# Kernel tuning notes

Measured on AMD Instinct MI355X. Metric: run time of the kernel, lower is better.

## Reference

```python
import jax, jax.numpy as jnp
import numpy as np

B, V, HP, WP = 1, 6, 37, 66
N, CD, CC = HP * WP, 768, 256
BEVH = BEVW = 100
Q = BEVH * BEVW
NH, NP, D, Z = 8, 4, 4, 8
HD = CC // NH
PC = (-51.2, -51.2, -5.0, 51.2, 51.2, 3.0)
SCALE, PT, PL = 0.5775, 0.0, 0.0
H2, W2 = 518, 924
EPS = 1e-6


def setup_inputs() -> dict:
    key = jax.random.key(0)
    ks = jax.random.split(key, 10)
    s = 0.02
    return {
        "last_tokens": jax.random.normal(ks[0], (B, V, N, CD), jnp.float32),
        "lidar2img": jax.random.normal(ks[1], (B, V, 4, 4), jnp.float32),
        "proj_w": jax.random.normal(ks[2], (CC, CD), jnp.float32) * s,
        "bev_query": jax.random.normal(ks[3], (Q, CC), jnp.float32) * s,
        "w_view": jnp.zeros((1, V, 1), jnp.float32),
        "vp_w": jax.random.normal(ks[4], (CC, CC), jnp.float32) * s,
        "vp_b": jnp.zeros((CC,), jnp.float32),
        "so_w": jax.random.normal(ks[5], (NH * NP * 2, CC), jnp.float32) * s,
        "so_b": jnp.zeros((NH * NP * 2,), jnp.float32),
        "aw_w": jax.random.normal(ks[6], (NH * NP, CC), jnp.float32) * s,
        "aw_b": jnp.zeros((NH * NP,), jnp.float32),
        "op_w": jax.random.normal(ks[7], (CC, CC), jnp.float32) * s,
        "op_b": jnp.zeros((CC,), jnp.float32),
    }


def _ref_points_3d():
    # normalized pillar reference points, (D, Q, 3) in xyz order, Q = h*BEVW + w
    xs = (jnp.arange(BEVW, dtype=jnp.float32) + 0.5) / BEVW
    ys = (jnp.arange(BEVH, dtype=jnp.float32) + 0.5) / BEVH
    zs = jnp.linspace(0.5, Z - 0.5, D, dtype=jnp.float32) / Z
    gx = jnp.broadcast_to(xs[None, :], (BEVH, BEVW)).reshape(-1)
    gy = jnp.broadcast_to(ys[:, None], (BEVH, BEVW)).reshape(-1)
    return jnp.stack([jnp.broadcast_to(gx, (D, Q)),
                      jnp.broadcast_to(gy, (D, Q)),
                      jnp.broadcast_to(zs[:, None], (D, Q))], axis=-1)


def reference(last_tokens, lidar2img, proj_w, bev_query, w_view,
              vp_w, vp_b, so_w, so_b, aw_w, aw_b, op_w, op_b):
    BV = B * V
    # ---- project 3D BEV pillar points to camera views ----
    ref = _ref_points_3d()  # (D, Q, 3)
    wx = ref[..., 0] * (PC[3] - PC[0]) + PC[0]
    wy = ref[..., 1] * (PC[4] - PC[1]) + PC[1]
    wz = ref[..., 2] * (PC[5] - PC[2]) + PC[2]
    ref4 = jnp.stack([wx, wy, wz, jnp.ones_like(wx)], axis=-1)  # (D, Q, 4)
    cam = jnp.einsum('bvij,dqj->bvdqi', lidar2img, ref4)  # (B, V, D, Q, 4)
    depth = cam[..., 2]
    bev_mask = depth > 1e-5
    uv = cam[..., :2] / jnp.clip(depth, 1e-5)[..., None]
    u = uv[..., 0] * SCALE + PL
    v = uv[..., 1] * SCALE + PT
    in_img = (u >= 0) & (u <= W2 - 1) & (v >= 0) & (v <= H2 - 1)
    valid = bev_mask & in_img
    refx = jnp.clip(u / max(W2 - 1.0, 1.0), 0.0, 1.0)
    refy = jnp.clip(v / max(H2 - 1.0, 1.0), 0.0, 1.0)
    w = jnp.maximum(valid.astype(jnp.float32), EPS)  # (B, V, D, Q)
    den = jnp.maximum(w.sum(2), EPS)
    rx = (refx * w).sum(2) / den
    ry = (refy * w).sum(2) / den
    ref2d = jnp.stack([rx, ry], axis=-1).reshape(BV, Q, 2)

    # ---- value features: 1x1 conv proj + value_proj ----
    val = jnp.einsum('bvnc,oc->bvno', last_tokens, proj_w).reshape(BV, N, CC)
    val = val @ vp_w.T + vp_b
    val = val.reshape(BV, N, NH, HD)

    # ---- deformable attention (single level) ----
    query = jnp.broadcast_to(bev_query[None], (BV, Q, CC))
    off = (query @ so_w.T + so_b).reshape(BV, Q, NH, NP, 2)
    attn = jax.nn.softmax((query @ aw_w.T + aw_b).reshape(BV, Q, NH, NP), axis=-1)
    normalizer = jnp.array([WP, HP], jnp.float32)
    loc = ref2d[:, :, None, None, :] + off / normalizer  # (BV, Q, NH, NP, 2)

    # bilinear sampling, grid_sample semantics (align_corners=False, zero pad)
    x = loc[..., 0] * WP - 0.5
    y = loc[..., 1] * HP - 0.5
    x0 = jnp.floor(x); y0 = jnp.floor(y)
    fx = x - x0; fy = y - y0
    x0i = x0.astype(jnp.int32); y0i = y0.astype(jnp.int32)
    b_idx = jnp.arange(BV)[:, None, None, None]
    h_idx = jnp.arange(NH)[None, None, :, None]

    def corner(xi, yi, wgt):
        ok = ((xi >= 0) & (xi < WP) & (yi >= 0) & (yi < HP)).astype(val.dtype)
        lin = jnp.clip(yi, 0, HP - 1) * WP + jnp.clip(xi, 0, WP - 1)
        g = val[b_idx, lin, h_idx]  # (BV, Q, NH, NP, HD)
        return g * (ok * wgt)[..., None]

    samp = (corner(x0i, y0i, (1 - fx) * (1 - fy))
            + corner(x0i + 1, y0i, fx * (1 - fy))
            + corner(x0i, y0i + 1, (1 - fx) * fy)
            + corner(x0i + 1, y0i + 1, fx * fy))
    out = (samp * attn[..., None]).sum(3).reshape(BV, Q, CC)
    out = out @ op_w.T + op_b + query  # residual (mmcv identity)

    # ---- view-weighted combine ----
    out = out.reshape(B, V, Q, CC)
    wv = jax.nn.softplus(w_view)  # (1, V, 1)
    num = (out * wv[..., None]).sum(1)  # (B, Q, CC)
    den_v = jnp.maximum(wv.sum(1), EPS)[..., None]
    bev = num / den_v
    return jnp.transpose(bev, (0, 2, 1)).reshape(B, CC, BEVH, BEVW)
```

## Files before the change

kernel.cpp:

```cpp
#include <hip/hip_runtime.h>
#include <math.h>

#define Q_TOT 10000
#define NVIEW 6
#define NTOK  2442
#define HP_   37
#define WP_   66
#define CD_   768
#define CC_   256

typedef __attribute__((ext_vector_type(8))) short bf16x8;
typedef __attribute__((ext_vector_type(4))) float f32x4;

__device__ inline unsigned f2bf(float f) {
    unsigned u = __builtin_bit_cast(unsigned, f);
    unsigned r = u + 0x7FFFu + ((u >> 16) & 1u);
    return r >> 16;
}

__global__ __launch_bounds__(256) void w2_kernel(const float* __restrict__ vp_w,
                                                 const float* __restrict__ proj_w,
                                                 unsigned short* __restrict__ W2b) {
    int b = blockIdx.x;
    int o2 = b / 3;
    int c = (b % 3) * 256 + threadIdx.x;
    __shared__ float vps[256];
    vps[threadIdx.x] = vp_w[(size_t)o2 * 256 + threadIdx.x];
    __syncthreads();
    float acc = 0.f;
#pragma unroll 16
    for (int o = 0; o < 256; ++o) {
        acc += vps[o] * proj_w[(size_t)o * CD_ + c];
    }
    W2b[(size_t)o2 * CD_ + c] = (unsigned short)f2bf(acc);
}

__global__ __launch_bounds__(256) void small_prep(const float* __restrict__ opw,
                                                  const float* __restrict__ l2i,
                                                  const float* __restrict__ so_w,
                                                  const float* __restrict__ so_b,
                                                  const float* __restrict__ aw_w,
                                                  const float* __restrict__ aw_b,
                                                  const float* __restrict__ wview,
                                                  unsigned short* __restrict__ opwb,
                                                  float* __restrict__ ref2d,
                                                  unsigned short* __restrict__ WQb,
                                                  float* __restrict__ bqp,
                                                  float* __restrict__ vwn) {
    int b = blockIdx.x, tid = threadIdx.x;
    if (b < 32) {
        int i = b * 256 + tid;
        float4 a = *(const float4*)(opw + (size_t)i * 8);
        float4 c4 = *(const float4*)(opw + (size_t)i * 8 + 4);
        uint4 o;
        o.x = f2bf(a.x) | (f2bf(a.y) << 16);
        o.y = f2bf(a.z) | (f2bf(a.w) << 16);
        o.z = f2bf(c4.x) | (f2bf(c4.y) << 16);
        o.w = f2bf(c4.z) | (f2bf(c4.w) << 16);
        *(uint4*)(opwb + (size_t)i * 8) = o;
    } else if (b < 267) {
        int idx = (b - 32) * 256 + tid;
        if (idx < NVIEW * Q_TOT) {
            int v = idx / Q_TOT, q = idx % Q_TOT;
            int wq = q % 100, hq = q / 100;
            float wx = (wq + 0.5f) * 1.024f - 51.2f;
            float wy = (hq + 0.5f) * 1.024f - 51.2f;
            const float* L = l2i + v * 16;
            float L0=L[0],L1=L[1],L2=L[2],L3=L[3],L4=L[4],L5=L[5],L6=L[6],L7=L[7];
            float L8=L[8],L9=L[9],L10=L[10],L11=L[11];
            float sw = 0.f, sx = 0.f, sy = 0.f;
#pragma unroll
            for (int d = 0; d < 4; ++d) {
                float zs = (0.5f + (float)d * (7.0f / 3.0f)) * 0.125f;
                float wz = zs * 8.0f - 5.0f;
                float c0 = L0 * wx + L1 * wy + L2 * wz + L3;
                float c1 = L4 * wx + L5 * wy + L6 * wz + L7;
                float c2 = L8 * wx + L9 * wy + L10 * wz + L11;
                bool bm = c2 > 1e-5f;
                float dc = fmaxf(c2, 1e-5f);
                float u  = (c0 / dc) * 0.5775f;
                float vv = (c1 / dc) * 0.5775f;
                bool in_img = (u >= 0.f) && (u <= 923.f) && (vv >= 0.f) && (vv <= 517.f);
                bool valid = bm && in_img;
                float refx = fminf(fmaxf(u / 923.0f, 0.f), 1.f);
                float refy = fminf(fmaxf(vv / 517.0f, 0.f), 1.f);
                float w = valid ? 1.0f : 1e-6f;
                sw += w; sx += refx * w; sy += refy * w;
            }
            float den = fmaxf(sw, 1e-6f);
            ref2d[(size_t)idx * 2 + 0] = sx / den;
            ref2d[(size_t)idx * 2 + 1] = sy / den;
        }
    } else {
        int row = b - 267, col = tid;
        float v = (row < 64) ? so_w[row * 256 + col] : (row < 96 ? aw_w[(row - 64) * 256 + col] : 0.f);
        WQb[row * 256 + col] = (unsigned short)f2bf(v);
        if (row == 0 && col < 128) bqp[col] = (col < 64) ? so_b[col] : (col < 96 ? aw_b[col - 64] : 0.f);
        if (row == 1 && col == 0) {
            float sp[6], swv = 0.f;
#pragma unroll
            for (int vv = 0; vv < NVIEW; ++vv) {
                float x = wview[vv];
                float s = (x > 20.f) ? x : log1pf(expf(x));
                sp[vv] = s; swv += s;
            }
            float inv = 1.0f / fmaxf(swv, 1e-6f);
#pragma unroll
            for (int vv = 0; vv < NVIEW; ++vv) vwn[vv] = sp[vv] * inv;
            vwn[6] = swv * inv;
            vwn[7] = 0.f;
        }
    }
}

template <int MODE, int KT>
__device__ __forceinline__ void gemm_body(char* base0, char* base1,
                                          const void* __restrict__ Aptr,
                                          const unsigned short* __restrict__ Bw,
                                          const float* __restrict__ bias,
                                          const float* __restrict__ resid,
                                          const float* __restrict__ wview,
                                          void* __restrict__ Cptr,
                                          int M, int nt_shift, int bid, int nwg) {
    constexpr int K = KT * 64;
    int tid = threadIdx.x;
    int wid = tid >> 6, lane = tid & 63;

    int qd = nwg >> 3, r = nwg & 7;
    int xcd = bid & 7, seq = bid >> 3;
    int wgid = (xcd < r) ? (xcd * (qd + 1) + seq) : (r * (qd + 1) + (xcd - r) * qd + seq);
    int mt = wgid >> nt_shift;
    int nt = wgid & ((1 << nt_shift) - 1);
    int m0 = mt * 64, n0 = nt * 64;

    int lr = lane & 15, lq = lane >> 4;
    int arow_s = tid >> 4;
    int ac4 = tid & 15;
    const float* Af = (const float*)Aptr;
    const unsigned short* Ah = (const unsigned short*)Aptr;
    float* Cf = (float*)Cptr;
    unsigned short* Ch = (unsigned short*)Cptr;

    f32x4 acc[4];
#pragma unroll
    for (int j = 0; j < 4; ++j) acc[j] = (f32x4)(0.f);

    float4 aF[2][4];
    uint4  aB[2][2];
    uint4  bR[2][2];
    const float4 zf4 = make_float4(0.f, 0.f, 0.f, 0.f);

#define LOADG(S, KTI) do {                                                            \
    int k0 = (KTI) << 6;                                                              \
    if (MODE == 0 || MODE == 2) {                                                     \
        _Pragma("unroll")                                                             \
        for (int p_ = 0; p_ < 4; ++p_) {                                              \
            int row_ = p_ * 16 + arow_s;                                              \
            bool av_ = (m0 + row_) < M;                                               \
            aF[S][p_] = av_ ? *(const float4*)(Af + (size_t)(m0 + row_) * K + k0 + ac4 * 4) : zf4; \
        }                                                                             \
    } else {                                                                          \
        _Pragma("unroll")                                                             \
        for (int i_ = 0; i_ < 2; ++i_) {                                              \
            int s_ = tid + (i_ << 8);                                                 \
            int row_ = s_ >> 3, c_ = s_ & 7;                                          \
            aB[S][i_] = *(const uint4*)(Ah + (size_t)(m0 + row_) * K + k0 + c_ * 8);  \
        }                                                                             \
    }                                                                                 \
    _Pragma("unroll")                                                                 \
    for (int i_ = 0; i_ < 2; ++i_) {                                                  \
        int s_ = tid + (i_ << 8);                                                     \
        int row_ = s_ >> 3, c_ = s_ & 7;                                              \
        bR[S][i_] = *(const uint4*)(Bw + (size_t)(n0 + row_) * K + k0 + c_ * 8);      \
    }                                                                                 \
} while (0)

#define TOLDS(S, PB) do {                                                             \
    char* Abb = (PB) ? base1 : base0;                                                 \
    if (MODE == 0 || MODE == 2) {                                                     \
        _Pragma("unroll")                                                             \
        for (int p_ = 0; p_ < 4; ++p_) {                                              \
            int row_ = p_ * 16 + arow_s;                                              \
            const float* f_ = (const float*)&aF[S][p_];                               \
            uint2 w_;                                                                 \
            w_.x = f2bf(f_[0]) | (f2bf(f_[1]) << 16);                                 \
            w_.y = f2bf(f_[2]) | (f2bf(f_[3]) << 16);                                 \
            int byte_ = row_ * 128 + (((ac4 >> 1) ^ (row_ & 7)) << 4) + ((ac4 & 1) << 3); \
            *(uint2*)(Abb + byte_) = w_;                                              \
        }                                                                             \
    } else {                                                                          \
        _Pragma("unroll")                                                             \
        for (int i_ = 0; i_ < 2; ++i_) {                                              \
            int s_ = tid + (i_ << 8);                                                 \
            int row_ = s_ >> 3, c_ = s_ & 7;                                          \
            *(uint4*)(Abb + row_ * 128 + ((c_ ^ (row_ & 7)) << 4)) = aB[S][i_];       \
        }                                                                             \
    }                                                                                 \
    char* Bbb = Abb + 8192;                                                           \
    _Pragma("unroll")                                                                 \
    for (int i_ = 0; i_ < 2; ++i_) {                                                  \
        int s_ = tid + (i_ << 8);                                                     \
        int row_ = s_ >> 3, c_ = s_ & 7;                                              \
        *(uint4*)(Bbb + row_ * 128 + ((c_ ^ (row_ & 7)) << 4)) = bR[S][i_];           \
    }                                                                                 \
} while (0)

#define MFMAS(PB) do {                                                                \
    char* Abb = (PB) ? base1 : base0;                                                 \
    char* Bbb = Abb + 8192;                                                           \
    _Pragma("unroll")                                                                 \
    for (int s_ = 0; s_ < 2; ++s_) {                                                  \
        int chunk_ = (s_ << 2) + lq;                                                  \
        int arow_ = (wid << 4) + lr;                                                  \
        bf16x8 af_ = *(bf16x8*)(Abb + arow_ * 128 + ((chunk_ ^ (arow_ & 7)) << 4));   \
        _Pragma("unroll")                                                             \
        for (int j_ = 0; j_ < 4; ++j_) {                                              \
            int brow_ = (j_ << 4) + lr;                                               \
            bf16x8 bf_ = *(bf16x8*)(Bbb + brow_ * 128 + ((chunk_ ^ (brow_ & 7)) << 4)); \
            acc[j_] = __builtin_amdgcn_mfma_f32_16x16x32_bf16(af_, bf_, acc[j_], 0, 0, 0); \
        }                                                                             \
    }                                                                                 \
} while (0)

#define BARRIER() do {                                                                \
    __builtin_amdgcn_sched_barrier(0);                                                \
    asm volatile("s_waitcnt lgkmcnt(0)" ::: "memory");                                \
    __builtin_amdgcn_s_barrier();                                                     \
    __builtin_amdgcn_sched_barrier(0);                                                \
} while (0)

    LOADG(0, 0);
#pragma unroll
    for (int kt = 0; kt < KT; ++kt) {
        if (kt + 1 < KT) LOADG((kt + 1) & 1, kt + 1);
        TOLDS(kt & 1, kt & 1);
        BARRIER();
        MFMAS(kt & 1);
    }

    int mb = m0 + (wid << 4) + (lq << 2);
    if (MODE == 0) {
#pragma unroll
        for (int j = 0; j < 4; ++j) {
            int n = n0 + (j << 4) + lr;
            float bn = bias[n];
#pragma unroll
            for (int e = 0; e < 4; ++e) {
                int m = mb + e;
                if (m < M) Ch[(size_t)m * 256 + n] = (unsigned short)f2bf(acc[j][e] + bn);
            }
        }
    } else if (MODE == 1) {
        float s = 0.f;
#pragma unroll
        for (int v = 0; v < 6; ++v) {
            float x = wview[v];
            s += (x > 20.f) ? x : log1pf(expf(x));
        }
        float f = s / fmaxf(s, 1e-6f);
#pragma unroll
        for (int j = 0; j < 4; ++j) {
            int n = n0 + (j << 4) + lr;
            float bn = bias[n];
            if (mb + 4 <= M) {
                float4 o;
                float* oo = (float*)&o;
#pragma unroll
                for (int e = 0; e < 4; ++e)
                    oo[e] = acc[j][e] + f * (bn + resid[(size_t)(mb + e) * 256 + n]);
                *(float4*)(Cf + (size_t)n * M + mb) = o;
            } else {
#pragma unroll
                for (int e = 0; e < 4; ++e) {
                    int m = mb + e;
                    if (m < M) Cf[(size_t)n * M + m] = acc[j][e] + f * (bn + resid[(size_t)m * 256 + n]);
                }
            }
        }
    } else {
#pragma unroll
        for (int j = 0; j < 4; ++j) {
            int n = n0 + (j << 4) + lr;
            if (n >= 96) continue;
            float bn = bias[n];
#pragma unroll
            for (int e = 0; e < 4; ++e) {
                int m = mb + e;
                if (m < M) Cf[(size_t)m * 96 + n] = acc[j][e] + bn;
            }
        }
    }
#undef LOADG
#undef TOLDS
#undef MFMAS
#undef BARRIER
}

__global__ __launch_bounds__(256, 4) void dual_gemm(const float* __restrict__ lt,
                                                    const unsigned short* __restrict__ W2b,
                                                    const float* __restrict__ vpb,
                                                    unsigned short* __restrict__ valB,
                                                    const float* __restrict__ bqq,
                                                    const unsigned short* __restrict__ WQb,
                                                    const float* __restrict__ bqp,
                                                    float* __restrict__ qout) {
    __shared__ unsigned short lds[4 * 64 * 64];
    char* b0 = (char*)lds;
    char* b1 = (char*)lds + 16384;
    if (blockIdx.x < 916)
        gemm_body<0, 12>(b0, b1, (const void*)lt, W2b, vpb, nullptr, nullptr,
                         (void*)valB, 14652, 2, blockIdx.x, 916);
    else
        gemm_body<2, 4>(b0, b1, (const void*)bqq, WQb, bqp, nullptr, nullptr,
                        (void*)qout, Q_TOT, 1, blockIdx.x - 916, 314);
}

__global__ __launch_bounds__(256, 4) void out_gemm(const unsigned short* __restrict__ sampavgB,
                                                   const unsigned short* __restrict__ opwb,
                                                   const float* __restrict__ opb,
                                                   const float* __restrict__ bqq,
                                                   const float* __restrict__ wview,
                                                   float* __restrict__ out) {
    __shared__ unsigned short lds[4 * 64 * 64];
    char* b0 = (char*)lds;
    char* b1 = (char*)lds + 16384;
    gemm_body<1, 4>(b0, b1, (const void*)sampavgB, opwb, opb, bqq, wview,
                    (void*)out, Q_TOT, 2, blockIdx.x, gridDim.x);
}

__global__ __launch_bounds__(256) void sample_kernel(const unsigned short* __restrict__ valB,
                                                     const float* __restrict__ ref2d,
                                                     const float* __restrict__ qout,
                                                     const float* __restrict__ vwn,
                                                     unsigned short* __restrict__ sampavgB) {
    __shared__ uint4  sOff[4 * 240];
    __shared__ float4 sW[4 * 240];
    __shared__ float4 sAt[4 * 8];
    __shared__ float  sVw[8];
    int tid = threadIdx.x;
    int qb = blockIdx.x * 4;

    if (tid < 32) {
        int ql = tid >> 3, h = tid & 7;
        const float* qo = qout + (size_t)(qb + ql) * 96 + 64 + h * 4;
        float a0 = qo[0], a1 = qo[1], a2 = qo[2], a3 = qo[3];
        float mx = fmaxf(fmaxf(a0, a1), fmaxf(a2, a3));
        float e0 = __expf(a0 - mx), e1 = __expf(a1 - mx), e2 = __expf(a2 - mx), e3 = __expf(a3 - mx);
        float inv = 1.0f / (e0 + e1 + e2 + e3);
        sAt[ql * 8 + h] = make_float4(e0 * inv, e1 * inv, e2 * inv, e3 * inv);
        if (tid < 8) sVw[tid] = vwn[tid < 6 ? tid : 0];
    }
    __syncthreads();

#pragma unroll
    for (int t = tid; t < 768; t += 256) {
        int ql = t / 192;
        int rem = t - ql * 192;
        int v = rem >> 5;
        int h = (rem >> 2) & 7;
        int p = rem & 3;
        int q = qb + ql;
        const float* qo = qout + (size_t)q * 96;
        float ox = qo[h * 8 + 2 * p];
        float oy = qo[h * 8 + 2 * p + 1];
        float at = ((const float*)&sAt[ql * 8 + h])[p];
        float scale = at * sVw[v];

        float rx = ref2d[(size_t)(v * Q_TOT + q) * 2 + 0];
        float ry = ref2d[(size_t)(v * Q_TOT + q) * 2 + 1];
        float x = rx * 66.0f + ox - 0.5f;
        float y = ry * 37.0f + oy - 0.5f;
        float xf = floorf(x), yf = floorf(y);
        float fx = x - xf, fy = y - yf;
        int xi = (int)xf, yi = (int)yf;

        float cw[4] = { (1.f - fx) * (1.f - fy), fx * (1.f - fy), (1.f - fx) * fy, fx * fy };
        unsigned off[4];
#pragma unroll
        for (int cyi = 0; cyi < 2; ++cyi) {
#pragma unroll
            for (int cxi = 0; cxi < 2; ++cxi) {
                int cx = xi + cxi, cy = yi + cyi;
                bool ok = (cx >= 0) && (cx < WP_) && (cy >= 0) && (cy < HP_);
                int ccx = cx < 0 ? 0 : (cx > WP_ - 1 ? WP_ - 1 : cx);
                int ccy = cy < 0 ? 0 : (cy > HP_ - 1 ? HP_ - 1 : cy);
                int c_ = cyi * 2 + cxi;
                off[c_] = (unsigned)((v * NTOK + ccy * WP_ + ccx) << 9);
                cw[c_] = ok ? cw[c_] * scale : 0.f;
            }
        }
        int slot = ql * 240 + v * 40 + h * 5 + p;
        sOff[slot] = make_uint4(off[0], off[1], off[2], off[3]);
        sW[slot]   = make_float4(cw[0], cw[1], cw[2], cw[3]);
    }
    __syncthreads();

    int ql = tid >> 6;
    int lane = tid & 63;
    int h = lane >> 3, d4 = (lane & 7) << 2;
    unsigned coff = (unsigned)((h * 32 + d4) << 1);
    const char* vbase = (const char*)valB;
    float acc0 = 0.f, acc1 = 0.f, acc2 = 0.f, acc3 = 0.f;
#pragma unroll
    for (int v = 0; v < NVIEW; ++v) {
#pragma unroll
        for (int p = 0; p < 4; ++p) {
            int slot = ql * 240 + v * 40 + h * 5 + p;
            uint4 off = sOff[slot];
            float4 w = sW[slot];
            uint2 r0 = *(const uint2*)(vbase + (off.x + coff));
            uint2 r1 = *(const uint2*)(vbase + (off.y + coff));
            uint2 r2 = *(const uint2*)(vbase + (off.z + coff));
            uint2 r3 = *(const uint2*)(vbase + (off.w + coff));
            float g0, g1;
            g0 = __builtin_bit_cast(float, r0.x << 16); g1 = __builtin_bit_cast(float, r0.x & 0xFFFF0000u);
            acc0 += w.x * g0; acc1 += w.x * g1;
            g0 = __builtin_bit_cast(float, r0.y << 16); g1 = __builtin_bit_cast(float, r0.y & 0xFFFF0000u);
            acc2 += w.x * g0; acc3 += w.x * g1;
            g0 = __builtin_bit_cast(float, r1.x << 16); g1 = __builtin_bit_cast(float, r1.x & 0xFFFF0000u);
            acc0 += w.y * g0; acc1 += w.y * g1;
            g0 = __builtin_bit_cast(float, r1.y << 16); g1 = __builtin_bit_cast(float, r1.y & 0xFFFF0000u);
            acc2 += w.y * g0; acc3 += w.y * g1;
            g0 = __builtin_bit_cast(float, r2.x << 16); g1 = __builtin_bit_cast(float, r2.x & 0xFFFF0000u);
            acc0 += w.z * g0; acc1 += w.z * g1;
            g0 = __builtin_bit_cast(float, r2.y << 16); g1 = __builtin_bit_cast(float, r2.y & 0xFFFF0000u);
            acc2 += w.z * g0; acc3 += w.z * g1;
            g0 = __builtin_bit_cast(float, r3.x << 16); g1 = __builtin_bit_cast(float, r3.x & 0xFFFF0000u);
            acc0 += w.w * g0; acc1 += w.w * g1;
            g0 = __builtin_bit_cast(float, r3.y << 16); g1 = __builtin_bit_cast(float, r3.y & 0xFFFF0000u);
            acc2 += w.w * g0; acc3 += w.w * g1;
        }
    }
    int q = qb + ql;
    unsigned u0 = f2bf(acc0) | (f2bf(acc1) << 16);
    unsigned u1 = f2bf(acc2) | (f2bf(acc3) << 16);
    *(uint2*)(sampavgB + (size_t)q * CC_ + h * 32 + d4) = make_uint2(u0, u1);
}

extern "C" void kernel_launch(void* const* d_in, const int* in_sizes, int n_in,
                              void* d_out, int out_size, void* d_ws, size_t ws_size,
                              hipStream_t stream) {
    const float* lt   = (const float*)d_in[0];
    const float* l2i  = (const float*)d_in[1];
    const float* proj = (const float*)d_in[2];
    const float* bqq  = (const float*)d_in[3];
    const float* wv   = (const float*)d_in[4];
    const float* vpw  = (const float*)d_in[5];
    const float* vpb  = (const float*)d_in[6];
    const float* sow  = (const float*)d_in[7];
    const float* sob  = (const float*)d_in[8];
    const float* aww  = (const float*)d_in[9];
    const float* awb  = (const float*)d_in[10];
    const float* opw  = (const float*)d_in[11];
    const float* opb  = (const float*)d_in[12];
    float* out = (float*)d_out;

    char* ws = (char*)d_ws;
    unsigned short* W2b   = (unsigned short*)(ws);
    unsigned short* opwb  = (unsigned short*)(ws + 393216);
    unsigned short* WQb   = (unsigned short*)(ws + 524288);
    float*          bqp   = (float*)(ws + 589824);
    float*          vwn   = (float*)(ws + 590336);
    float*          ref2d = (float*)(ws + 590848);
    float*          qout  = (float*)(ws + 1070848);
    unsigned short* valB  = (unsigned short*)(ws + 4910848);
    unsigned short* sampavgB = (unsigned short*)(ws + 12412672);

    hipLaunchKernelGGL(w2_kernel, dim3(768), dim3(256), 0, stream, vpw, proj, W2b);
    hipLaunchKernelGGL(small_prep, dim3(395), dim3(256), 0, stream,
                       opw, l2i, sow, sob, aww, awb, wv, opwb, ref2d, WQb, bqp, vwn);
    hipLaunchKernelGGL(dual_gemm, dim3(1230), dim3(256), 0, stream,
                       lt, W2b, vpb, valB, bqq, WQb, bqp, qout);
    hipLaunchKernelGGL(sample_kernel, dim3(Q_TOT / 4), dim3(256), 0, stream,
                       valB, ref2d, qout, vwn, sampavgB);
    hipLaunchKernelGGL(out_gemm, dim3(628), dim3(256), 0, stream,
                       sampavgB, opwb, opb, bqq, wv, out);
}
```

Baseline: 87.18 us.

## Use 128-row M tiles for the token projection GEMM in dual_gemm

```diff
diff --git a/kernel.cpp b/kernel.cpp
--- a/kernel.cpp
+++ b/kernel.cpp
@@ -113,6 +113,142 @@
     }
 }
 
+template <int KT>
+__device__ __forceinline__ void gemm_body128(char* base0, char* base1,
+                                             const float* __restrict__ Af,
+                                             const unsigned short* __restrict__ Bw,
+                                             const float* __restrict__ bias,
+                                             unsigned short* __restrict__ Ch,
+                                             int M, int bid, int nwg) {
+    constexpr int K = KT * 64;
+    int tid = threadIdx.x;
+    int wid = tid >> 6, lane = tid & 63;
+
+    int qd = nwg >> 3, r = nwg & 7;
+    int xcd = bid & 7, seq = bid >> 3;
+    int wgid = (xcd < r) ? (xcd * (qd + 1) + seq) : (r * (qd + 1) + (xcd - r) * qd + seq);
+    int mt = wgid >> 2;
+    int nt = wgid & 3;
+    int m0 = mt * 128, n0 = nt * 64;
+
+    int lr = lane & 15, lq = lane >> 4;
+    int arow_h = tid >> 2;
+    int af4 = (tid & 3) * 4;
+
+    f32x4 acc[2][4];
+#pragma unroll
+    for (int i = 0; i < 2; ++i)
+#pragma unroll
+        for (int j = 0; j < 4; ++j) acc[i][j] = (f32x4)(0.f);
+
+    float4 aF[2][2][4];
+    uint4  bR[2][2];
+    const float4 zf4 = make_float4(0.f, 0.f, 0.f, 0.f);
+
+#define LOADG1(S, KTI) do {                                                           \
+    int k0 = (KTI) << 6;                                                              \
+    _Pragma("unroll")                                                                 \
+    for (int p_ = 0; p_ < 2; ++p_) {                                                  \
+        int row_ = p_ * 64 + arow_h;                                                  \
+        bool av_ = (m0 + row_) < M;                                                   \
+        const float* ap = Af + (size_t)(m0 + row_) * K + k0 + af4 * 4;                \
+        aF[S][p_][0] = av_ ? *(const float4*)(ap + 0)  : zf4;                         \
+        aF[S][p_][1] = av_ ? *(const float4*)(ap + 4)  : zf4;                         \
+        aF[S][p_][2] = av_ ? *(const float4*)(ap + 8)  : zf4;                         \
+        aF[S][p_][3] = av_ ? *(const float4*)(ap + 12) : zf4;                         \
+    }                                                                                 \
+    _Pragma("unroll")                                                                 \
+    for (int i_ = 0; i_ < 2; ++i_) {                                                  \
+        int s_ = tid + (i_ << 8);                                                     \
+        int row_ = s_ >> 3, c_ = s_ & 7;                                              \
+        bR[S][i_] = *(const uint4*)(Bw + (size_t)(n0 + row_) * K + ((KTI) << 6) + c_ * 8); \
+    }                                                                                 \
+} while (0)
+
+#define TOLDS1(S, PB) do {                                                            \
+    char* Abb = (PB) ? base1 : base0;                                                 \
+    _Pragma("unroll")                                                                 \
+    for (int p_ = 0; p_ < 2; ++p_) {                                                  \
+        int row_ = p_ * 64 + arow_h;                                                  \
+        const float* f_ = (const float*)&aF[S][p_][0];                                \
+        unsigned u_[8];                                                               \
+        _Pragma("unroll")                                                             \
+        for (int k_ = 0; k_ < 4; ++k_) {                                              \
+            u_[2 * k_]     = f2bf(f_[4 * k_ + 0]) | (f2bf(f_[4 * k_ + 1]) << 16);     \
+            u_[2 * k_ + 1] = f2bf(f_[4 * k_ + 2]) | (f2bf(f_[4 * k_ + 3]) << 16);     \
+        }                                                                             \
+        int cb_ = (tid & 3) * 2;                                                      \
+        *(uint4*)(Abb + row_ * 128 + (((cb_) ^ (row_ & 7)) << 4))     = make_uint4(u_[0], u_[1], u_[2], u_[3]); \
+        *(uint4*)(Abb + row_ * 128 + (((cb_ + 1) ^ (row_ & 7)) << 4)) = make_uint4(u_[4], u_[5], u_[6], u_[7]); \
+    }                                                                                 \
+    char* Bbb = Abb + 16384;                                                          \
+    _Pragma("unroll")                                                                 \
+    for (int i_ = 0; i_ < 2; ++i_) {                                                  \
+        int s_ = tid + (i_ << 8);                                                     \
+        int row_ = s_ >> 3, c_ = s_ & 7;                                              \
+        *(uint4*)(Bbb + row_ * 128 + ((c_ ^ (row_ & 7)) << 4)) = bR[S][i_];           \
+    }                                                                                 \
+} while (0)
+
+#define MFMAS1(PB) do {                                                               \
+    char* Abb = (PB) ? base1 : base0;                                                 \
+    char* Bbb = Abb + 16384;                                                          \
+    _Pragma("unroll")                                                                 \
+    for (int s_ = 0; s_ < 2; ++s_) {                                                  \
+        int chunk_ = (s_ << 2) + lq;                                                  \
+        bf16x8 af0_, af1_;                                                            \
+        {                                                                             \
+            int ar0_ = (wid << 5) + lr;                                               \
+            int ar1_ = (wid << 5) + 16 + lr;                                          \
+            af0_ = *(bf16x8*)(Abb + ar0_ * 128 + ((chunk_ ^ (ar0_ & 7)) << 4));       \
+            af1_ = *(bf16x8*)(Abb + ar1_ * 128 + ((chunk_ ^ (ar1_ & 7)) << 4));       \
+        }                                                                             \
+        _Pragma("unroll")                                                             \
+        for (int j_ = 0; j_ < 4; ++j_) {                                              \
+            int brow_ = (j_ << 4) + lr;                                               \
+            bf16x8 bf_ = *(bf16x8*)(Bbb + brow_ * 128 + ((chunk_ ^ (brow_ & 7)) << 4)); \
+            acc[0][j_] = __builtin_amdgcn_mfma_f32_16x16x32_bf16(af0_, bf_, acc[0][j_], 0, 0, 0); \
+            acc[1][j_] = __builtin_amdgcn_mfma_f32_16x16x32_bf16(af1_, bf_, acc[1][j_], 0, 0, 0); \
+        }                                                                             \
+    }                                                                                 \
+} while (0)
+
+#define BARRIER1() do {                                                               \
+    __builtin_amdgcn_sched_barrier(0);                                                \
+    asm volatile("s_waitcnt lgkmcnt(0)" ::: "memory");                                \
+    __builtin_amdgcn_s_barrier();                                                     \
+    __builtin_amdgcn_sched_barrier(0);                                                \
+} while (0)
+
+    LOADG1(0, 0);
+#pragma unroll
+    for (int kt = 0; kt < KT; ++kt) {
+        if (kt + 1 < KT) LOADG1((kt + 1) & 1, kt + 1);
+        TOLDS1(kt & 1, kt & 1);
+        BARRIER1();
+        MFMAS1(kt & 1);
+    }
+
+#pragma unroll
+    for (int i = 0; i < 2; ++i) {
+        int mb = m0 + (wid << 5) + (i << 4) + (lq << 2);
+#pragma unroll
+        for (int j = 0; j < 4; ++j) {
+            int n = n0 + (j << 4) + lr;
+            float bn = bias[n];
+#pragma unroll
+            for (int e = 0; e < 4; ++e) {
+                int m = mb + e;
+                if (m < M) Ch[(size_t)m * 256 + n] = (unsigned short)f2bf(acc[i][j][e] + bn);
+            }
+        }
+    }
+#undef LOADG1
+#undef TOLDS1
+#undef MFMAS1
+#undef BARRIER1
+}
+
 template <int MODE, int KT>
 __device__ __forceinline__ void gemm_body(char* base0, char* base1,
                                           const void* __restrict__ Aptr,
@@ -139,7 +275,6 @@
     const float* Af = (const float*)Aptr;
     const unsigned short* Ah = (const unsigned short*)Aptr;
     float* Cf = (float*)Cptr;
-    unsigned short* Ch = (unsigned short*)Cptr;
 
     f32x4 acc[4];
 #pragma unroll
@@ -152,7 +287,7 @@
 
 #define LOADG(S, KTI) do {                                                            \
     int k0 = (KTI) << 6;                                                              \
-    if (MODE == 0 || MODE == 2) {                                                     \
+    if (MODE == 2) {                                                                  \
         _Pragma("unroll")                                                             \
         for (int p_ = 0; p_ < 4; ++p_) {                                              \
             int row_ = p_ * 16 + arow_s;                                              \
@@ -177,7 +312,7 @@
 
 #define TOLDS(S, PB) do {                                                             \
     char* Abb = (PB) ? base1 : base0;                                                 \
-    if (MODE == 0 || MODE == 2) {                                                     \
+    if (MODE == 2) {                                                                  \
         _Pragma("unroll")                                                             \
         for (int p_ = 0; p_ < 4; ++p_) {                                              \
             int row_ = p_ * 16 + arow_s;                                              \
@@ -239,18 +374,7 @@
     }
 
     int mb = m0 + (wid << 4) + (lq << 2);
-    if (MODE == 0) {
-#pragma unroll
-        for (int j = 0; j < 4; ++j) {
-            int n = n0 + (j << 4) + lr;
-            float bn = bias[n];
-#pragma unroll
-            for (int e = 0; e < 4; ++e) {
-                int m = mb + e;
-                if (m < M) Ch[(size_t)m * 256 + n] = (unsigned short)f2bf(acc[j][e] + bn);
-            }
-        }
-    } else if (MODE == 1) {
+    if (MODE == 1) {
         float s = 0.f;
 #pragma unroll
         for (int v = 0; v < 6; ++v) {
@@ -296,7 +420,7 @@
 #undef BARRIER
 }
 
-__global__ __launch_bounds__(256, 4) void dual_gemm(const float* __restrict__ lt,
+__global__ __launch_bounds__(256, 3) void dual_gemm(const float* __restrict__ lt,
                                                     const unsigned short* __restrict__ W2b,
                                                     const float* __restrict__ vpb,
                                                     unsigned short* __restrict__ valB,
@@ -304,15 +428,12 @@
                                                     const unsigned short* __restrict__ WQb,
                                                     const float* __restrict__ bqp,
                                                     float* __restrict__ qout) {
-    __shared__ unsigned short lds[4 * 64 * 64];
-    char* b0 = (char*)lds;
-    char* b1 = (char*)lds + 16384;
-    if (blockIdx.x < 916)
-        gemm_body<0, 12>(b0, b1, (const void*)lt, W2b, vpb, nullptr, nullptr,
-                         (void*)valB, 14652, 2, blockIdx.x, 916);
+    __shared__ char lds[49152];
+    if (blockIdx.x < 460)
+        gemm_body128<12>(lds, lds + 24576, lt, W2b, vpb, valB, 14652, blockIdx.x, 460);
     else
-        gemm_body<2, 4>(b0, b1, (const void*)bqq, WQb, bqp, nullptr, nullptr,
-                        (void*)qout, Q_TOT, 1, blockIdx.x - 916, 314);
+        gemm_body<2, 4>(lds, lds + 16384, (const void*)bqq, WQb, bqp, nullptr, nullptr,
+                        (void*)qout, Q_TOT, 1, blockIdx.x - 460, 314);
 }
 
 __global__ __launch_bounds__(256, 4) void out_gemm(const unsigned short* __restrict__ sampavgB,
@@ -321,10 +442,8 @@
                                                    const float* __restrict__ bqq,
                                                    const float* __restrict__ wview,
                                                    float* __restrict__ out) {
-    __shared__ unsigned short lds[4 * 64 * 64];
-    char* b0 = (char*)lds;
-    char* b1 = (char*)lds + 16384;
-    gemm_body<1, 4>(b0, b1, (const void*)sampavgB, opwb, opb, bqq, wview,
+    __shared__ char lds[32768];
+    gemm_body<1, 4>(lds, lds + 16384, (const void*)sampavgB, opwb, opb, bqq, wview,
                     (void*)out, Q_TOT, 2, blockIdx.x, gridDim.x);
 }
 
@@ -469,7 +588,7 @@
     hipLaunchKernelGGL(w2_kernel, dim3(768), dim3(256), 0, stream, vpw, proj, W2b);
     hipLaunchKernelGGL(small_prep, dim3(395), dim3(256), 0, stream,
                        opw, l2i, sow, sob, aww, awb, wv, opwb, ref2d, WQb, bqp, vwn);
-    hipLaunchKernelGGL(dual_gemm, dim3(1230), dim3(256), 0, stream,
+    hipLaunchKernelGGL(dual_gemm, dim3(774), dim3(256), 0, stream,
                        lt, W2b, vpb, valB, bqq, WQb, bqp, qout);
     hipLaunchKernelGGL(sample_kernel, dim3(Q_TOT / 4), dim3(256), 0, stream,
                        valB, ref2d, qout, vwn, sampavgB);
```

Result: slower. 158.9 us (+82.3%).

## Merge prep kernels and deepen GEMM global prefetch to three stages

Applied to the files above, without the earlier changes.

```diff
diff --git a/kernel.cpp b/kernel.cpp
--- a/kernel.cpp
+++ b/kernel.cpp
@@ -18,36 +18,37 @@
     return r >> 16;
 }
 
-__global__ __launch_bounds__(256) void w2_kernel(const float* __restrict__ vp_w,
-                                                 const float* __restrict__ proj_w,
-                                                 unsigned short* __restrict__ W2b) {
-    int b = blockIdx.x;
-    int o2 = b / 3;
-    int c = (b % 3) * 256 + threadIdx.x;
-    __shared__ float vps[256];
-    vps[threadIdx.x] = vp_w[(size_t)o2 * 256 + threadIdx.x];
-    __syncthreads();
-    float acc = 0.f;
+__global__ __launch_bounds__(256) void prep_all(const float* __restrict__ vp_w,
+                                                const float* __restrict__ proj_w,
+                                                const float* __restrict__ opw,
+                                                const float* __restrict__ l2i,
+                                                const float* __restrict__ so_w,
+                                                const float* __restrict__ so_b,
+                                                const float* __restrict__ aw_w,
+                                                const float* __restrict__ aw_b,
+                                                const float* __restrict__ wview,
+                                                unsigned short* __restrict__ W2b,
+                                                unsigned short* __restrict__ opwb,
+                                                float* __restrict__ ref2d,
+                                                unsigned short* __restrict__ WQb,
+                                                float* __restrict__ bqp,
+                                                float* __restrict__ vwn) {
+    int b0 = blockIdx.x, tid = threadIdx.x;
+    if (b0 < 768) {
+        int o2 = b0 / 3;
+        int c = (b0 % 3) * 256 + tid;
+        __shared__ float vps[256];
+        vps[tid] = vp_w[(size_t)o2 * 256 + tid];
+        __syncthreads();
+        float acc = 0.f;
 #pragma unroll 16
-    for (int o = 0; o < 256; ++o) {
-        acc += vps[o] * proj_w[(size_t)o * CD_ + c];
-    }
-    W2b[(size_t)o2 * CD_ + c] = (unsigned short)f2bf(acc);
-}
-
-__global__ __launch_bounds__(256) void small_prep(const float* __restrict__ opw,
-                                                  const float* __restrict__ l2i,
-                                                  const float* __restrict__ so_w,
-                                                  const float* __restrict__ so_b,
-                                                  const float* __restrict__ aw_w,
-                                                  const float* __restrict__ aw_b,
-                                                  const float* __restrict__ wview,
-                                                  unsigned short* __restrict__ opwb,
-                                                  float* __restrict__ ref2d,
-                                                  unsigned short* __restrict__ WQb,
-                                                  float* __restrict__ bqp,
-                                                  float* __restrict__ vwn) {
-    int b = blockIdx.x, tid = threadIdx.x;
+        for (int o = 0; o < 256; ++o) {
+            acc += vps[o] * proj_w[(size_t)o * CD_ + c];
+        }
+        W2b[(size_t)o2 * CD_ + c] = (unsigned short)f2bf(acc);
+        return;
+    }
+    int b = b0 - 768;
     if (b < 32) {
         int i = b * 256 + tid;
         float4 a = *(const float4*)(opw + (size_t)i * 8);
@@ -145,9 +146,9 @@
 #pragma unroll
     for (int j = 0; j < 4; ++j) acc[j] = (f32x4)(0.f);
 
-    float4 aF[2][4];
-    uint4  aB[2][2];
-    uint4  bR[2][2];
+    float4 aF[3][4];
+    uint4  aB[3][2];
+    uint4  bR[3][2];
     const float4 zf4 = make_float4(0.f, 0.f, 0.f, 0.f);
 
 #define LOADG(S, KTI) do {                                                            \
@@ -230,10 +231,12 @@
 } while (0)
 
     LOADG(0, 0);
+    if (KT > 1) LOADG(1, 1);
+    if (KT > 2) LOADG(2, 2);
 #pragma unroll
     for (int kt = 0; kt < KT; ++kt) {
-        if (kt + 1 < KT) LOADG((kt + 1) & 1, kt + 1);
-        TOLDS(kt & 1, kt & 1);
+        TOLDS(kt % 3, kt & 1);
+        if (kt + 3 < KT) LOADG(kt % 3, kt + 3);
         BARRIER();
         MFMAS(kt & 1);
     }
@@ -296,7 +299,7 @@
 #undef BARRIER
 }
 
-__global__ __launch_bounds__(256, 4) void dual_gemm(const float* __restrict__ lt,
+__global__ __launch_bounds__(256, 3) void dual_gemm(const float* __restrict__ lt,
                                                     const unsigned short* __restrict__ W2b,
                                                     const float* __restrict__ vpb,
                                                     unsigned short* __restrict__ valB,
@@ -315,7 +318,7 @@
                         (void*)qout, Q_TOT, 1, blockIdx.x - 916, 314);
 }
 
-__global__ __launch_bounds__(256, 4) void out_gemm(const unsigned short* __restrict__ sampavgB,
+__global__ __launch_bounds__(256, 3) void out_gemm(const unsigned short* __restrict__ sampavgB,
                                                    const unsigned short* __restrict__ opwb,
                                                    const float* __restrict__ opb,
                                                    const float* __restrict__ bqq,
@@ -466,9 +469,9 @@
     unsigned short* valB  = (unsigned short*)(ws + 4910848);
     unsigned short* sampavgB = (unsigned short*)(ws + 12412672);
 
-    hipLaunchKernelGGL(w2_kernel, dim3(768), dim3(256), 0, stream, vpw, proj, W2b);
-    hipLaunchKernelGGL(small_prep, dim3(395), dim3(256), 0, stream,
-                       opw, l2i, sow, sob, aww, awb, wv, opwb, ref2d, WQb, bqp, vwn);
+    hipLaunchKernelGGL(prep_all, dim3(1163), dim3(256), 0, stream,
+                       vpw, proj, opw, l2i, sow, sob, aww, awb, wv,
+                       W2b, opwb, ref2d, WQb, bqp, vwn);
     hipLaunchKernelGGL(dual_gemm, dim3(1230), dim3(256), 0, stream,
                        lt, W2b, vpb, valB, bqq, WQb, bqp, qout);
     hipLaunchKernelGGL(sample_kernel, dim3(Q_TOT / 4), dim3(256), 0, stream,
```

New measurement: 85.86 us. No clear change (-1.5%).

## Pre-convert tokens to bf16 and stage GEMM tiles via direct global-to-LDS loads

Applied to the files above, without the earlier changes.

```diff
diff --git a/kernel.cpp b/kernel.cpp
--- a/kernel.cpp
+++ b/kernel.cpp
@@ -18,38 +18,62 @@
     return r >> 16;
 }
 
-__global__ __launch_bounds__(256) void w2_kernel(const float* __restrict__ vp_w,
-                                                 const float* __restrict__ proj_w,
-                                                 unsigned short* __restrict__ W2b) {
-    int b = blockIdx.x;
-    int o2 = b / 3;
-    int c = (b % 3) * 256 + threadIdx.x;
-    __shared__ float vps[256];
-    vps[threadIdx.x] = vp_w[(size_t)o2 * 256 + threadIdx.x];
-    __syncthreads();
-    float acc = 0.f;
+__device__ __forceinline__ void glds16(const void* g, void* l) {
+    __builtin_amdgcn_global_load_lds(
+        (const __attribute__((address_space(1))) unsigned int*)g,
+        (__attribute__((address_space(3))) unsigned int*)l,
+        16, 0, 0);
+}
+
+__global__ __launch_bounds__(256) void prep_all(const float* __restrict__ lt,
+                                                const float* __restrict__ vp_w,
+                                                const float* __restrict__ proj_w,
+                                                const float* __restrict__ opw,
+                                                const float* __restrict__ l2i,
+                                                const float* __restrict__ so_w,
+                                                const float* __restrict__ so_b,
+                                                const float* __restrict__ aw_w,
+                                                const float* __restrict__ aw_b,
+                                                const float* __restrict__ wview,
+                                                unsigned short* __restrict__ ltB,
+                                                unsigned short* __restrict__ W2b,
+                                                unsigned short* __restrict__ opwb,
+                                                float* __restrict__ ref2d,
+                                                unsigned short* __restrict__ WQb,
+                                                float* __restrict__ bqp,
+                                                float* __restrict__ vwn) {
+    int b0 = blockIdx.x, tid = threadIdx.x;
+    if (b0 < 5495) {
+        int i = b0 * 256 + tid;
+        if (i < 1406592) {
+            float4 a = *(const float4*)(lt + (size_t)i * 8);
+            float4 c4 = *(const float4*)(lt + (size_t)i * 8 + 4);
+            uint4 o;
+            o.x = f2bf(a.x) | (f2bf(a.y) << 16);
+            o.y = f2bf(a.z) | (f2bf(a.w) << 16);
+            o.z = f2bf(c4.x) | (f2bf(c4.y) << 16);
+            o.w = f2bf(c4.z) | (f2bf(c4.w) << 16);
+            *(uint4*)(ltB + (size_t)i * 8) = o;
+        }
+        return;
+    }
+    if (b0 < 6263) {
+        int b = b0 - 5495;
+        int o2 = b / 3;
+        int c = (b % 3) * 256 + tid;
+        __shared__ float vps[256];
+        vps[tid] = vp_w[(size_t)o2 * 256 + tid];
+        __syncthreads();
+        float acc = 0.f;
 #pragma unroll 16
-    for (int o = 0; o < 256; ++o) {
-        acc += vps[o] * proj_w[(size_t)o * CD_ + c];
-    }
-    W2b[(size_t)o2 * CD_ + c] = (unsigned short)f2bf(acc);
-}
-
-__global__ __launch_bounds__(256) void small_prep(const float* __restrict__ opw,
-                                                  const float* __restrict__ l2i,
-                                                  const float* __restrict__ so_w,
-                                                  const float* __restrict__ so_b,
-                                                  const float* __restrict__ aw_w,
-                                                  const float* __restrict__ aw_b,
-                                                  const float* __restrict__ wview,
-                                                  unsigned short* __restrict__ opwb,
-                                                  float* __restrict__ ref2d,
-                                                  unsigned short* __restrict__ WQb,
-                                                  float* __restrict__ bqp,
-                                                  float* __restrict__ vwn) {
-    int b = blockIdx.x, tid = threadIdx.x;
-    if (b < 32) {
-        int i = b * 256 + tid;
+        for (int o = 0; o < 256; ++o) {
+            acc += vps[o] * proj_w[(size_t)o * CD_ + c];
+        }
+        W2b[(size_t)o2 * CD_ + c] = (unsigned short)f2bf(acc);
+        return;
+    }
+    if (b0 < 6295) {
+        int i = (b0 - 6263) * 256 + tid;
         float4 a = *(const float4*)(opw + (size_t)i * 8);
         float4 c4 = *(const float4*)(opw + (size_t)i * 8 + 4);
         uint4 o;
@@ -58,8 +82,10 @@
         o.z = f2bf(c4.x) | (f2bf(c4.y) << 16);
         o.w = f2bf(c4.z) | (f2bf(c4.w) << 16);
         *(uint4*)(opwb + (size_t)i * 8) = o;
-    } else if (b < 267) {
-        int idx = (b - 32) * 256 + tid;
+        return;
+    }
+    if (b0 < 6530) {
+        int idx = (b0 - 6295) * 256 + tid;
         if (idx < NVIEW * Q_TOT) {
             int v = idx / Q_TOT, q = idx % Q_TOT;
             int wq = q % 100, hq = q / 100;
@@ -91,8 +117,10 @@
             ref2d[(size_t)idx * 2 + 0] = sx / den;
             ref2d[(size_t)idx * 2 + 1] = sy / den;
         }
-    } else {
-        int row = b - 267, col = tid;
+        return;
+    }
+    {
+        int row = b0 - 6530, col = tid;
         float v = (row < 64) ? so_w[row * 256 + col] : (row < 96 ? aw_w[(row - 64) * 256 + col] : 0.f);
         WQb[row * 256 + col] = (unsigned short)f2bf(v);
         if (row == 0 && col < 128) bqp[col] = (col < 64) ? so_b[col] : (col < 96 ? aw_b[col - 64] : 0.f);
@@ -114,8 +142,8 @@
 }
 
 template <int MODE, int KT>
-__device__ __forceinline__ void gemm_body(char* base0, char* base1,
-                                          const void* __restrict__ Aptr,
+__device__ __forceinline__ void gemm_glds(char* base0, char* base1,
+                                          const unsigned short* __restrict__ Ah,
                                           const unsigned short* __restrict__ Bw,
                                           const float* __restrict__ bias,
                                           const float* __restrict__ resid,
@@ -134,10 +162,6 @@
     int m0 = mt * 64, n0 = nt * 64;
 
     int lr = lane & 15, lq = lane >> 4;
-    int arow_s = tid >> 4;
-    int ac4 = tid & 15;
-    const float* Af = (const float*)Aptr;
-    const unsigned short* Ah = (const unsigned short*)Aptr;
     float* Cf = (float*)Cptr;
     unsigned short* Ch = (unsigned short*)Cptr;
 
@@ -145,67 +169,26 @@
 #pragma unroll
     for (int j = 0; j < 4; ++j) acc[j] = (f32x4)(0.f);
 
-    float4 aF[2][4];
-    uint4  aB[2][2];
-    uint4  bR[2][2];
-    const float4 zf4 = make_float4(0.f, 0.f, 0.f, 0.f);
-
-#define LOADG(S, KTI) do {                                                            \
-    int k0 = (KTI) << 6;                                                              \
-    if (MODE == 0 || MODE == 2) {                                                     \
-        _Pragma("unroll")                                                             \
-        for (int p_ = 0; p_ < 4; ++p_) {                                              \
-            int row_ = p_ * 16 + arow_s;                                              \
-            bool av_ = (m0 + row_) < M;                                               \
-            aF[S][p_] = av_ ? *(const float4*)(Af + (size_t)(m0 + row_) * K + k0 + ac4 * 4) : zf4; \
-        }                                                                             \
-    } else {                                                                          \
-        _Pragma("unroll")                                                             \
-        for (int i_ = 0; i_ < 2; ++i_) {                                              \
-            int s_ = tid + (i_ << 8);                                                 \
-            int row_ = s_ >> 3, c_ = s_ & 7;                                          \
-            aB[S][i_] = *(const uint4*)(Ah + (size_t)(m0 + row_) * K + k0 + c_ * 8);  \
-        }                                                                             \
-    }                                                                                 \
+#define STAGE(PB, KTI) do {                                                           \
+    char* buf = (PB) ? base1 : base0;                                                 \
+    int k0b = (KTI) << 7;                                                             \
     _Pragma("unroll")                                                                 \
     for (int i_ = 0; i_ < 2; ++i_) {                                                  \
-        int s_ = tid + (i_ << 8);                                                     \
-        int row_ = s_ >> 3, c_ = s_ & 7;                                              \
-        bR[S][i_] = *(const uint4*)(Bw + (size_t)(n0 + row_) * K + k0 + c_ * 8);      \
+        int L_ = tid + (i_ << 8);                                                     \
+        int row_ = L_ >> 3, c_ = L_ & 7;                                              \
+        glds16((const char*)Ah + (size_t)(m0 + row_) * (K * 2) + k0b + ((c_ ^ (row_ & 7)) << 4), \
+               buf + (L_ << 4));                                                      \
+    }                                                                                 \
+    _Pragma("unroll")                                                                 \
+    for (int i_ = 0; i_ < 2; ++i_) {                                                  \
+        int L_ = tid + (i_ << 8);                                                     \
+        int row_ = L_ >> 3, c_ = L_ & 7;                                              \
+        glds16((const char*)Bw + (size_t)(n0 + row_) * (K * 2) + k0b + ((c_ ^ (row_ & 7)) << 4), \
+               buf + 8192 + (L_ << 4));                                               \
     }                                                                                 \
 } while (0)
 
-#define TOLDS(S, PB) do {                                                             \
-    char* Abb = (PB) ? base1 : base0;                                                 \
-    if (MODE == 0 || MODE == 2) {                                                     \
-        _Pragma("unroll")                                                             \
-        for (int p_ = 0; p_ < 4; ++p_) {                                              \
-            int row_ = p_ * 16 + arow_s;                                              \
-            const float* f_ = (const float*)&aF[S][p_];                               \
-            uint2 w_;                                                                 \
-            w_.x = f2bf(f_[0]) | (f2bf(f_[1]) << 16);                                 \
-            w_.y = f2bf(f_[2]) | (f2bf(f_[3]) << 16);                                 \
-            int byte_ = row_ * 128 + (((ac4 >> 1) ^ (row_ & 7)) << 4) + ((ac4 & 1) << 3); \
-            *(uint2*)(Abb + byte_) = w_;                                              \
-        }                                                                             \
-    } else {                                                                          \
-        _Pragma("unroll")                                                             \
-        for (int i_ = 0; i_ < 2; ++i_) {                                              \
-            int s_ = tid + (i_ << 8);                                                 \
-            int row_ = s_ >> 3, c_ = s_ & 7;                                          \
-            *(uint4*)(Abb + row_ * 128 + ((c_ ^ (row_ & 7)) << 4)) = aB[S][i_];       \
-        }                                                                             \
-    }                                                                                 \
-    char* Bbb = Abb + 8192;                                                           \
-    _Pragma("unroll")                                                                 \
-    for (int i_ = 0; i_ < 2; ++i_) {                                                  \
-        int s_ = tid + (i_ << 8);                                                     \
-        int row_ = s_ >> 3, c_ = s_ & 7;                                              \
-        *(uint4*)(Bbb + row_ * 128 + ((c_ ^ (row_ & 7)) << 4)) = bR[S][i_];           \
-    }                                                                                 \
-} while (0)
-
-#define MFMAS(PB) do {                                                                \
+#define GMFMA(PB) do {                                                                \
     char* Abb = (PB) ? base1 : base0;                                                 \
     char* Bbb = Abb + 8192;                                                           \
     _Pragma("unroll")                                                                 \
@@ -222,20 +205,18 @@
     }                                                                                 \
 } while (0)
 
-#define BARRIER() do {                                                                \
-    __builtin_amdgcn_sched_barrier(0);                                                \
-    asm volatile("s_waitcnt lgkmcnt(0)" ::: "memory");                                \
-    __builtin_amdgcn_s_barrier();                                                     \
-    __builtin_amdgcn_sched_barrier(0);                                                \
-} while (0)
-
-    LOADG(0, 0);
+    STAGE(0, 0);
+    asm volatile("s_waitcnt vmcnt(0)" ::: "memory");
+    __builtin_amdgcn_s_barrier();
+    __builtin_amdgcn_sched_barrier(0);
 #pragma unroll
     for (int kt = 0; kt < KT; ++kt) {
-        if (kt + 1 < KT) LOADG((kt + 1) & 1, kt + 1);
-        TOLDS(kt & 1, kt & 1);
-        BARRIER();
-        MFMAS(kt & 1);
+        if (kt + 1 < KT) STAGE((kt + 1) & 1, kt + 1);
+        GMFMA(kt & 1);
+        __builtin_amdgcn_sched_barrier(0);
+        asm volatile("s_waitcnt vmcnt(0)" ::: "memory");
+        __builtin_amdgcn_s_barrier();
+        __builtin_amdgcn_sched_barrier(0);
     }
 
     int mb = m0 + (wid << 4) + (lq << 2);
@@ -250,7 +231,7 @@
                 if (m < M) Ch[(size_t)m * 256 + n] = (unsigned short)f2bf(acc[j][e] + bn);
             }
         }
-    } else if (MODE == 1) {
+    } else {
         float s = 0.f;
 #pragma unroll
         for (int v = 0; v < 6; ++v) {
@@ -277,26 +258,125 @@
                 }
             }
         }
-    } else {
-#pragma unroll
-        for (int j = 0; j < 4; ++j) {
-            int n = n0 + (j << 4) + lr;
-            if (n >= 96) continue;
-            float bn = bias[n];
-#pragma unroll
-            for (int e = 0; e < 4; ++e) {
-                int m = mb + e;
-                if (m < M) Cf[(size_t)m * 96 + n] = acc[j][e] + bn;
-            }
-        }
-    }
-#undef LOADG
-#undef TOLDS
-#undef MFMAS
-#undef BARRIER
-}
-
-__global__ __launch_bounds__(256, 4) void dual_gemm(const float* __restrict__ lt,
+    }
+#undef STAGE
+#undef GMFMA
+}
+
+template <int KT>
+__device__ __forceinline__ void gemm_f32A(char* base0, char* base1,
+                                          const float* __restrict__ Af,
+                                          const unsigned short* __restrict__ Bw,
+                                          const float* __restrict__ bias,
+                                          float* __restrict__ Cf,
+                                          int M, int nt_shift, int bid, int nwg) {
+    constexpr int K = KT * 64;
+    int tid = threadIdx.x;
+    int wid = tid >> 6, lane = tid & 63;
+
+    int qd = nwg >> 3, r = nwg & 7;
+    int xcd = bid & 7, seq = bid >> 3;
+    int wgid = (xcd < r) ? (xcd * (qd + 1) + seq) : (r * (qd + 1) + (xcd - r) * qd + seq);
+    int mt = wgid >> nt_shift;
+    int nt = wgid & ((1 << nt_shift) - 1);
+    int m0 = mt * 64, n0 = nt * 64;
+
+    int lr = lane & 15, lq = lane >> 4;
+    int arow_s = tid >> 4;
+    int ac4 = tid & 15;
+
+    f32x4 acc[4];
+#pragma unroll
+    for (int j = 0; j < 4; ++j) acc[j] = (f32x4)(0.f);
+
+    float4 aF[2][4];
+    uint4  bR[2][2];
+    const float4 zf4 = make_float4(0.f, 0.f, 0.f, 0.f);
+
+#define QLOADG(S, KTI) do {                                                           \
+    int k0 = (KTI) << 6;                                                              \
+    _Pragma("unroll")                                                                 \
+    for (int p_ = 0; p_ < 4; ++p_) {                                                  \
+        int row_ = p_ * 16 + arow_s;                                                  \
+        bool av_ = (m0 + row_) < M;                                                   \
+        aF[S][p_] = av_ ? *(const float4*)(Af + (size_t)(m0 + row_) * K + k0 + ac4 * 4) : zf4; \
+    }                                                                                 \
+    _Pragma("unroll")                                                                 \
+    for (int i_ = 0; i_ < 2; ++i_) {                                                  \
+        int s_ = tid + (i_ << 8);                                                     \
+        int row_ = s_ >> 3, c_ = s_ & 7;                                              \
+        bR[S][i_] = *(const uint4*)(Bw + (size_t)(n0 + row_) * K + k0 + c_ * 8);      \
+    }                                                                                 \
+} while (0)
+
+#define QTOLDS(S, PB) do {                                                            \
+    char* Abb = (PB) ? base1 : base0;                                                 \
+    _Pragma("unroll")                                                                 \
+    for (int p_ = 0; p_ < 4; ++p_) {                                                  \
+        int row_ = p_ * 16 + arow_s;                                                  \
+        const float* f_ = (const float*)&aF[S][p_];                                   \
+        uint2 w_;                                                                     \
+        w_.x = f2bf(f_[0]) | (f2bf(f_[1]) << 16);                                     \
+        w_.y = f2bf(f_[2]) | (f2bf(f_[3]) << 16);                                     \
+        int byte_ = row_ * 128 + (((ac4 >> 1) ^ (row_ & 7)) << 4) + ((ac4 & 1) << 3); \
+        *(uint2*)(Abb + byte_) = w_;                                                  \
+    }                                                                                 \
+    char* Bbb = Abb + 8192;                                                           \
+    _Pragma("unroll")                                                                 \
+    for (int i_ = 0; i_ < 2; ++i_) {                                                  \
+        int s_ = tid + (i_ << 8);                                                     \
+        int row_ = s_ >> 3, c_ = s_ & 7;                                              \
+        *(uint4*)(Bbb + row_ * 128 + ((c_ ^ (row_ & 7)) << 4)) = bR[S][i_];           \
+    }                                                                                 \
+} while (0)
+
+#define QMFMAS(PB) do {                                                               \
+    char* Abb = (PB) ? base1 : base0;                                                 \
+    char* Bbb = Abb + 8192;                                                           \
+    _Pragma("unroll")                                                                 \
+    for (int s_ = 0; s_ < 2; ++s_) {                                                  \
+        int chunk_ = (s_ << 2) + lq;                                                  \
+        int arow_ = (wid << 4) + lr;                                                  \
+        bf16x8 af_ = *(bf16x8*)(Abb + arow_ * 128 + ((chunk_ ^ (arow_ & 7)) << 4));   \
+        _Pragma("unroll")                                                             \
+        for (int j_ = 0; j_ < 4; ++j_) {                                              \
+            int brow_ = (j_ << 4) + lr;                                               \
+            bf16x8 bf_ = *(bf16x8*)(Bbb + brow_ * 128 + ((chunk_ ^ (brow_ & 7)) << 4)); \
+            acc[j_] = __builtin_amdgcn_mfma_f32_16x16x32_bf16(af_, bf_, acc[j_], 0, 0, 0); \
+        }                                                                             \
+    }                                                                                 \
+} while (0)
+
+    QLOADG(0, 0);
+#pragma unroll
+    for (int kt = 0; kt < KT; ++kt) {
+        if (kt + 1 < KT) QLOADG((kt + 1) & 1, kt + 1);
+        QTOLDS(kt & 1, kt & 1);
+        __builtin_amdgcn_sched_barrier(0);
+        asm volatile("s_waitcnt lgkmcnt(0)" ::: "memory");
+        __builtin_amdgcn_s_barrier();
+        __builtin_amdgcn_sched_barrier(0);
+        QMFMAS(kt & 1);
+    }
+
+    int mb = m0 + (wid << 4) + (lq << 2);
+#pragma unroll
+    for (int j = 0; j < 4; ++j) {
+        int n = n0 + (j << 4) + lr;
+        if (n >= 96) continue;
+        float bn = bias[n];
+#pragma unroll
+        for (int e = 0; e < 4; ++e) {
+            int m = mb + e;
+            if (m < M) Cf[(size_t)m * 96 + n] = acc[j][e] + bn;
+        }
+    }
+#undef QLOADG
+#undef QTOLDS
+#undef QMFMAS
+}
+
+__global__ __launch_bounds__(256, 4) void dual_gemm(const unsigned short* __restrict__ ltB,
                                                     const unsigned short* __restrict__ W2b,
                                                     const float* __restrict__ vpb,
                                                     unsigned short* __restrict__ valB,
@@ -304,15 +384,14 @@
                                                     const unsigned short* __restrict__ WQb,
                                                     const float* __restrict__ bqp,
                                                     float* __restrict__ qout) {
-    __shared__ unsigned short lds[4 * 64 * 64];
-    char* b0 = (char*)lds;
-    char* b1 = (char*)lds + 16384;
+    __shared__ char lds[32768];
+    char* b0 = lds;
+    char* b1 = lds + 16384;
     if (blockIdx.x < 916)
-        gemm_body<0, 12>(b0, b1, (const void*)lt, W2b, vpb, nullptr, nullptr,
+        gemm_glds<0, 12>(b0, b1, ltB, W2b, vpb, nullptr, nullptr,
                          (void*)valB, 14652, 2, blockIdx.x, 916);
     else
-        gemm_body<2, 4>(b0, b1, (const void*)bqq, WQb, bqp, nullptr, nullptr,
-                        (void*)qout, Q_TOT, 1, blockIdx.x - 916, 314);
+        gemm_f32A<4>(b0, b1, bqq, WQb, bqp, qout, Q_TOT, 1, blockIdx.x - 916, 314);
 }
 
 __global__ __launch_bounds__(256, 4) void out_gemm(const unsigned short* __restrict__ sampavgB,
@@ -321,10 +400,8 @@
                                                    const float* __restrict__ bqq,
                                                    const float* __restrict__ wview,
                                                    float* __restrict__ out) {
-    __shared__ unsigned short lds[4 * 64 * 64];
-    char* b0 = (char*)lds;
-    char* b1 = (char*)lds + 16384;
-    gemm_body<1, 4>(b0, b1, (const void*)sampavgB, opwb, opb, bqq, wview,
+    __shared__ char lds[32768];
+    gemm_glds<1, 4>(lds, lds + 16384, sampavgB, opwb, opb, bqq, wview,
                     (void*)out, Q_TOT, 2, blockIdx.x, gridDim.x);
 }
 
@@ -464,13 +541,14 @@
     float*          ref2d = (float*)(ws + 590848);
     float*          qout  = (float*)(ws + 1070848);
     unsigned short* valB  = (unsigned short*)(ws + 4910848);
+    unsigned short* ltB   = (unsigned short*)(ws + 12412672);
     unsigned short* sampavgB = (unsigned short*)(ws + 12412672);
 
-    hipLaunchKernelGGL(w2_kernel, dim3(768), dim3(256), 0, stream, vpw, proj, W2b);
-    hipLaunchKernelGGL(small_prep, dim3(395), dim3(256), 0, stream,
-                       opw, l2i, sow, sob, aww, awb, wv, opwb, ref2d, WQb, bqp, vwn);
+    hipLaunchKernelGGL(prep_all, dim3(6658), dim3(256), 0, stream,
+                       lt, vpw, proj, opw, l2i, sow, sob, aww, awb, wv,
+                       ltB, W2b, opwb, ref2d, WQb, bqp, vwn);
     hipLaunchKernelGGL(dual_gemm, dim3(1230), dim3(256), 0, stream,
-                       lt, W2b, vpb, valB, bqq, WQb, bqp, qout);
+                       ltB, W2b, vpb, valB, bqq, WQb, bqp, qout);
     hipLaunchKernelGGL(sample_kernel, dim3(Q_TOT / 4), dim3(256), 0, stream,
                        valB, ref2d, qout, vwn, sampavgB);
     hipLaunchKernelGGL(out_gemm, dim3(628), dim3(256), 0, stream,
```

Measured after the change: 95.18 us. 9.2% more time.
